# Performance work log

Hardware: AMD Instinct MI355X
Metric: run time of the kernel (lower is better)

The kernel has to match this reference:

```python
import jax, jax.numpy as jnp
import numpy as np

D_MODEL = 1024
D_STATE = 32
EXPAND = 2
D_INNER = D_MODEL * EXPAND
B_SZ = 2
SEQ = 512


def setup_inputs() -> dict:
    key = jax.random.key(0)
    ks = jax.random.split(key, 10)
    x = jax.random.normal(ks[0], (B_SZ, SEQ, D_MODEL), dtype=jnp.float32)
    W_in = jax.random.normal(ks[1], (2 * D_INNER, D_MODEL), dtype=jnp.float32) * 0.02
    A_log = jax.random.uniform(ks[2], (D_INNER, D_STATE), minval=-4.0, maxval=-1.0, dtype=jnp.float32)
    W_B = jax.random.normal(ks[3], (D_STATE, D_MODEL), dtype=jnp.float32) * 0.02
    W_C = jax.random.normal(ks[4], (D_STATE, D_MODEL), dtype=jnp.float32) * 0.02
    W_dt = jax.random.normal(ks[5], (D_INNER, D_MODEL), dtype=jnp.float32) * 0.02
    b_dt = jnp.zeros((D_INNER,), dtype=jnp.float32)
    dt_bias = jnp.zeros((D_INNER,), dtype=jnp.float32) - 4.0
    rope_freq = jax.random.normal(ks[6], (D_STATE // 2,), dtype=jnp.float32) * 0.01
    ln_w = jnp.ones((D_INNER,), dtype=jnp.float32)
    ln_b = jnp.zeros((D_INNER,), dtype=jnp.float32)
    W_out = jax.random.normal(ks[7], (D_MODEL, D_INNER), dtype=jnp.float32) * 0.02
    return {"x": x, "W_in": W_in, "A_log": A_log, "W_B": W_B, "W_C": W_C,
            "W_dt": W_dt, "b_dt": b_dt, "dt_bias": dt_bias, "rope_freq": rope_freq,
            "ln_w": ln_w, "ln_b": ln_b, "W_out": W_out}


def _forward(x, W_in, A_log, W_B, W_C, W_dt, b_dt, dt_bias, rope_freq, ln_w, ln_b, W_out):
    B, L, _ = x.shape
    half = D_STATE // 2
    offset = 0

    xz = jnp.einsum('bld,ed->ble', x, W_in)                 # [B,L,2*D_INNER]
    x_inner = xz[..., :D_INNER]                             # [B,L,DI]
    z = jax.nn.silu(xz[..., D_INNER:])                      # [B,L,DI]

    A = -jnp.exp(A_log)                                     # [DI,DS]
    Bm = jnp.einsum('bld,nd->bln', x, W_B)                  # [B,L,DS]
    Cm = jnp.einsum('bld,nd->bln', x, W_C)                  # [B,L,DS]
    dt = jax.nn.softplus(jnp.einsum('bld,ed->ble', x, W_dt) + b_dt + dt_bias)  # [B,L,DI]

    # trapezoidal discretization
    dtA = dt[..., None] * A                                 # [B,L,DI,DS]
    denom = 1.0 - dtA / 2.0
    A_bar = (1.0 + dtA / 2.0) / denom                       # [B,L,DI,DS]
    B_bar = dt[..., None] / denom                           # [B,L,DI,DS]

    # per-step rope rotation angles: angle_t = rope_freq * (t + offset)
    t_idx = jnp.arange(L, dtype=jnp.float32) + offset       # [L]
    ang = t_idx[:, None] * rope_freq                        # [L,half]
    cos_a = jnp.cos(ang)
    sin_a = jnp.sin(ang)

    def step(state, inp):
        A_t, Bb_t, B_t, x_t, C_t, c_t, s_t = inp
        # state update: [B,DI,DS]
        state = A_t * state + Bb_t * B_t[:, None, :] * x_t[:, :, None]
        real = state[..., :half]
        imag = state[..., half:]
        state = jnp.concatenate([real * c_t - imag * s_t,
                                 real * s_t + imag * c_t], axis=-1)
        y_t = jnp.einsum('bds,bs->bd', state, C_t)          # [B,DI]
        return state, y_t

    state0 = jnp.zeros((B, D_INNER, D_STATE), dtype=x.dtype)
    xs = (jnp.swapaxes(A_bar, 0, 1), jnp.swapaxes(B_bar, 0, 1),
          jnp.swapaxes(Bm, 0, 1), jnp.swapaxes(x_inner, 0, 1),
          jnp.swapaxes(Cm, 0, 1), cos_a, sin_a)
    final_state, ys = jax.lax.scan(step, state0, xs)        # ys: [L,B,DI]
    out = jnp.swapaxes(ys, 0, 1) * z                        # [B,L,DI]

    # LayerNorm over last dim (eps=1e-5, torch default)
    mu = jnp.mean(out, axis=-1, keepdims=True)
    var = jnp.mean((out - mu) ** 2, axis=-1, keepdims=True)
    out = (out - mu) * jax.lax.rsqrt(var + 1e-5) * ln_w + ln_b

    out = jnp.einsum('ble,de->bld', out, W_out)             # [B,L,D_MODEL]
    return out, final_state


def reference(x, W_in, A_log, W_B, W_C, W_dt, b_dt, dt_bias, rope_freq, ln_w, ln_b, W_out):
    return _forward(x, W_in, A_log, W_B, W_C, W_dt, b_dt, dt_bias, rope_freq, ln_w, ln_b, W_out)
```

## Files before the change

kernel.cpp:

```cpp
#include <hip/hip_runtime.h>
#include <math.h>

#define B_SZ 2
#define SEQ 512
#define DM 1024
#define DI 2048
#define DS 32
#define TOK (B_SZ*SEQ)
#define NCH 8
#define CLEN (SEQ/NCH)
#define NG (CLEN/4)
#define NPAIR (B_SZ*DI*16)

#define NFUSED 6272

__device__ __forceinline__ unsigned short f2bf(float f) {
  unsigned int u = __builtin_bit_cast(unsigned int, f);
  unsigned int r = u + 0x7fffu + ((u >> 16) & 1u);
  return (unsigned short)(r >> 16);
}

template<int CTRL>
__device__ __forceinline__ float row_ror_add(float x) {
  int s = __builtin_amdgcn_update_dpp(0, __builtin_bit_cast(int, x), CTRL, 0xf, 0xf, false);
  return x + __builtin_bit_cast(float, s);
}
__device__ __forceinline__ float row16_sum(float v) {
  v = row_ror_add<0x121>(v);
  v = row_ror_add<0x122>(v);
  v = row_ror_add<0x124>(v);
  v = row_ror_add<0x128>(v);
  return v;
}

__global__ __launch_bounds__(256) void fused_cast(const float* __restrict__ x,
                                                  const float* __restrict__ W_in,
                                                  const float* __restrict__ W_dt,
                                                  const float* __restrict__ W_B,
                                                  const float* __restrict__ W_C,
                                                  const float* __restrict__ W_out,
                                                  unsigned short* __restrict__ xb,
                                                  unsigned short* __restrict__ wcat,
                                                  unsigned short* __restrict__ wob) {
  int g = blockIdx.x * 256 + threadIdx.x;
  const float* s; unsigned short* dd; int off;
  if      (g <  131072) { s = x;     dd = xb;             off = 0; }
  else if (g <  655360) { s = W_in;  dd = wcat;           off = 131072; }
  else if (g <  917504) { s = W_dt;  dd = wcat + 4194304; off = 655360; }
  else if (g <  921600) { s = W_B;   dd = wcat + 6291456; off = 917504; }
  else if (g <  925696) { s = W_C;   dd = wcat + 6324224; off = 921600; }
  else if (g < 1187840) { s = W_out; dd = wob;            off = 925696; }
  else return;
  int i = g - off;
  float4 a = ((const float4*)s)[i * 2];
  float4 b = ((const float4*)s)[i * 2 + 1];
  union { unsigned short us[8]; uint4 v; } o;
  o.us[0] = f2bf(a.x); o.us[1] = f2bf(a.y); o.us[2] = f2bf(a.z); o.us[3] = f2bf(a.w);
  o.us[4] = f2bf(b.x); o.us[5] = f2bf(b.y); o.us[6] = f2bf(b.z); o.us[7] = f2bf(b.w);
  ((uint4*)dd)[i] = o.v;
}

typedef __attribute__((ext_vector_type(8))) short  frag8;
typedef __attribute__((ext_vector_type(4))) float  facc4;

__device__ __forceinline__ void gload_lds16(const unsigned short* g, unsigned short* l) {
  __builtin_amdgcn_global_load_lds((const __attribute__((address_space(1))) unsigned int*)g,
                                   (__attribute__((address_space(3))) unsigned int*)l, 16, 0, 0);
}

__device__ __forceinline__ float softplus_fast(float v) {
  return fmaxf(v, 0.f) + __logf(1.f + __expf(-fabsf(v)));
}

template<int BMt, int BNt, int MT, bool ROUTE>
__global__ __launch_bounds__(256) void gemm_mfma(const unsigned short* __restrict__ A,
                                                 const unsigned short* __restrict__ Bw,
                                                 int K,
                                                 float* __restrict__ o_xs,
                                                 float* __restrict__ o_zb,
                                                 float* __restrict__ o_dts,
                                                 float* __restrict__ o_bcb,
                                                 const float* __restrict__ b_dt,
                                                 const float* __restrict__ dt_bias,
                                                 float* __restrict__ o_c, int ldc) {
  constexpr int FM = BMt / 32, FN = BNt / 32;
  constexpr int IA = BMt / 64, IB = BNt / 64;
  __shared__ __align__(16) unsigned short As[BMt * 32];
  __shared__ __align__(16) unsigned short Bs[BNt * 32];
  const int tid = threadIdx.x;
  const int w = tid >> 6, lane = tid & 63;
  const int wm = w >> 1, wn = w & 1;
  const int bid = blockIdx.x;
  const int Wk = (bid & 7) * ((int)gridDim.x >> 3) + (bid >> 3);
  const int m0 = (Wk % MT) * BMt;
  const int n0 = (Wk / MT) * BNt;
  const int r = lane & 15, q = lane >> 4;
  const int grow = lane >> 2, gk = (lane & 3) * 8;
  facc4 acc[FM][FN] = {};
  const unsigned short* Ag = A + (size_t)m0 * K + gk;
  const unsigned short* Bg = Bw + (size_t)n0 * K + gk;

  for (int k0 = 0; k0 < K; k0 += 32) {
#pragma unroll
    for (int i = 0; i < IA; ++i) {
      int ch = i * 4 + w;
      gload_lds16(Ag + (size_t)(ch * 16 + grow) * K + k0, &As[ch * 512]);
    }
#pragma unroll
    for (int i = 0; i < IB; ++i) {
      int ch = i * 4 + w;
      gload_lds16(Bg + (size_t)(ch * 16 + grow) * K + k0, &Bs[ch * 512]);
    }
    __syncthreads();
    frag8 af[FM], bf[FN];
#pragma unroll
    for (int i = 0; i < FM; ++i)
      af[i] = *(const frag8*)&As[(wm * (BMt / 2) + i * 16 + r) * 32 + q * 8];
#pragma unroll
    for (int jj = 0; jj < FN; ++jj)
      bf[jj] = *(const frag8*)&Bs[(wn * (BNt / 2) + jj * 16 + r) * 32 + q * 8];
#pragma unroll
    for (int i = 0; i < FM; ++i)
#pragma unroll
      for (int jj = 0; jj < FN; ++jj)
        acc[i][jj] = __builtin_amdgcn_mfma_f32_16x16x32_bf16(af[i], bf[jj], acc[i][jj], 0, 0, 0);
    __syncthreads();
  }

#pragma unroll
  for (int i = 0; i < FM; ++i) {
#pragma unroll
    for (int jj = 0; jj < FN; ++jj) {
      int n = n0 + wn * (BNt / 2) + jj * 16 + r;
      int mb = m0 + wm * (BMt / 2) + i * 16 + q * 4;
      if (ROUTE) {
        if (n < 2048) {
#pragma unroll
          for (int rg = 0; rg < 4; ++rg)
            o_xs[(size_t)(mb + rg) * DI + n] = acc[i][jj][rg];
        } else if (n < 4096) {
#pragma unroll
          for (int rg = 0; rg < 4; ++rg)
            o_zb[(size_t)(mb + rg) * DI + (n - 2048)] = acc[i][jj][rg];
        } else if (n < 6144) {
          int d = n - 4096;
          float bias = b_dt[d] + dt_bias[d];
#pragma unroll
          for (int rg = 0; rg < 4; ++rg)
            o_dts[(size_t)(mb + rg) * DI + d] = softplus_fast(acc[i][jj][rg] + bias);
        } else if (n < 6176) {
#pragma unroll
          for (int rg = 0; rg < 4; ++rg)
            o_bcb[(size_t)(mb + rg) * DS + (n - 6144)] = acc[i][jj][rg];
        } else if (n < 6208) {
#pragma unroll
          for (int rg = 0; rg < 4; ++rg)
            o_bcb[(size_t)TOK * DS + (size_t)(mb + rg) * DS + (n - 6176)] = acc[i][jj][rg];
        }
      } else {
#pragma unroll
        for (int rg = 0; rg < 4; ++rg)
          o_c[(size_t)(mb + rg) * ldc + n] = acc[i][jj][rg];
      }
    }
  }
}


__global__ __launch_bounds__(256) void scan_p1(const float* __restrict__ xs,
                                               const float* __restrict__ dts,
                                               const float* __restrict__ bcb,
                                               const float* __restrict__ A_log,
                                               const float* __restrict__ rope,
                                               float* __restrict__ Pbuf) {
  const int blk = blockIdx.x;
  const int c = blk >> 7;
  const int sub = blk & 127;
  const int b = sub >> 6;
  const int dbase = (sub & 63) << 5;
  const int dl = threadIdx.x >> 4;
  const int j = threadIdx.x & 15;
  const int dA = dbase + dl;
  const int dB = dA + 16;
  const int l0 = c * CLEN;

  const float ArA = -0.5f * expf(A_log[dA * DS + j]);
  const float AiA = -0.5f * expf(A_log[dA * DS + j + 16]);
  const float ArB = -0.5f * expf(A_log[dB * DS + j]);
  const float AiB = -0.5f * expf(A_log[dB * DS + j + 16]);
  const float fr = rope[j];
  float sn, cs, sF, cF;
  sincosf((float)l0 * fr, &sn, &cs);
  sincosf(fr, &sF, &cF);

  const size_t base = (size_t)(b * SEQ + l0);
  const float* dtpA = dts + base * DI + dA;
  const float* xpA  = xs  + base * DI + dA;
  const float* Brp  = bcb + base * DS + j;
  const float* Bip  = Brp + 16;

  float p00A = 1.f, p01A = 0.f, p10A = 0.f, p11A = 1.f, urA = 0.f, uiA = 0.f;
  float p00B = 1.f, p01B = 0.f, p10B = 0.f, p11B = 1.f, urB = 0.f, uiB = 0.f;

  float cdtA[4], cdtB[4], cxA[4], cxB[4], cbr[4], cbi[4];
#pragma unroll
  for (int t = 0; t < 4; ++t) {
    cdtA[t] = dtpA[t * DI]; cdtB[t] = dtpA[t * DI + 16];
    cxA[t]  = xpA[t * DI];  cxB[t]  = xpA[t * DI + 16];
    cbr[t]  = Brp[t * DS];  cbi[t]  = Bip[t * DS];
  }

  for (int g = 0; g < NG; ++g) {
    const int gb = ((g + 1 < NG) ? g + 1 : g) * 4;
    float ndtA[4], ndtB[4], nxA[4], nxB[4], nbr[4], nbi[4];
#pragma unroll
    for (int t = 0; t < 4; ++t) {
      ndtA[t] = dtpA[(gb + t) * DI]; ndtB[t] = dtpA[(gb + t) * DI + 16];
      nxA[t]  = xpA[(gb + t) * DI];  nxB[t]  = xpA[(gb + t) * DI + 16];
      nbr[t]  = Brp[(gb + t) * DS];  nbi[t]  = Bip[(gb + t) * DS];
    }
#pragma unroll
    for (int t = 0; t < 4; ++t) {
      const float Br = cbr[t], Bi = cbi[t];
      {
        float dtd = cdtA[t];
        float hr = dtd * ArA, hi = dtd * AiA;
        float invr = __builtin_amdgcn_rcpf(1.f - hr);
        float invi = __builtin_amdgcn_rcpf(1.f - hi);
        float Abr = (1.f + hr) * invr;
        float Abi = (1.f + hi) * invi;
        float dx = dtd * cxA[t];
        float bxr = dx * invr * Br;
        float bxi = dx * invi * Bi;
        float tr = fmaf(Abr, urA, bxr);
        float ti = fmaf(Abi, uiA, bxi);
        urA = tr * cs - ti * sn;
        uiA = tr * sn + ti * cs;
        float q00 = Abr * p00A, q01 = Abr * p01A;
        float q10 = Abi * p10A, q11 = Abi * p11A;
        p00A = q00 * cs - q10 * sn; p10A = q00 * sn + q10 * cs;
        p01A = q01 * cs - q11 * sn; p11A = q01 * sn + q11 * cs;
      }
      {
        float dtd = cdtB[t];
        float hr = dtd * ArB, hi = dtd * AiB;
        float invr = __builtin_amdgcn_rcpf(1.f - hr);
        float invi = __builtin_amdgcn_rcpf(1.f - hi);
        float Abr = (1.f + hr) * invr;
        float Abi = (1.f + hi) * invi;
        float dx = dtd * cxB[t];
        float bxr = dx * invr * Br;
        float bxi = dx * invi * Bi;
        float tr = fmaf(Abr, urB, bxr);
        float ti = fmaf(Abi, uiB, bxi);
        urB = tr * cs - ti * sn;
        uiB = tr * sn + ti * cs;
        float q00 = Abr * p00B, q01 = Abr * p01B;
        float q10 = Abi * p10B, q11 = Abi * p11B;
        p00B = q00 * cs - q10 * sn; p10B = q00 * sn + q10 * cs;
        p01B = q01 * cs - q11 * sn; p11B = q01 * sn + q11 * cs;
      }
      float nc = fmaf(cs, cF, -sn * sF);
      float ns = fmaf(sn, cF,  cs * sF);
      cs = nc; sn = ns;
    }
#pragma unroll
    for (int t = 0; t < 4; ++t) {
      cdtA[t] = ndtA[t]; cdtB[t] = ndtB[t]; cxA[t] = nxA[t]; cxB[t] = nxB[t];
      cbr[t] = nbr[t]; cbi[t] = nbi[t];
    }
  }
  const int pairA = (b * DI + dA) * 16 + j;
  const int pairB = (b * DI + dB) * 16 + j;
  Pbuf[(c * 6 + 0) * NPAIR + pairA] = p00A;
  Pbuf[(c * 6 + 1) * NPAIR + pairA] = p01A;
  Pbuf[(c * 6 + 2) * NPAIR + pairA] = p10A;
  Pbuf[(c * 6 + 3) * NPAIR + pairA] = p11A;
  Pbuf[(c * 6 + 4) * NPAIR + pairA] = urA;
  Pbuf[(c * 6 + 5) * NPAIR + pairA] = uiA;
  Pbuf[(c * 6 + 0) * NPAIR + pairB] = p00B;
  Pbuf[(c * 6 + 1) * NPAIR + pairB] = p01B;
  Pbuf[(c * 6 + 2) * NPAIR + pairB] = p10B;
  Pbuf[(c * 6 + 3) * NPAIR + pairB] = p11B;
  Pbuf[(c * 6 + 4) * NPAIR + pairB] = urB;
  Pbuf[(c * 6 + 5) * NPAIR + pairB] = uiB;
}

__global__ __launch_bounds__(256) void scan_p3(const float* __restrict__ xs,
                                               const float* __restrict__ dts,
                                               const float* __restrict__ bcb,
                                               const float* __restrict__ A_log,
                                               const float* __restrict__ rope,
                                               const float* __restrict__ Pbuf,
                                               float* __restrict__ y,
                                               float* __restrict__ fstate) {
  const int blk = blockIdx.x;
  const int c = blk >> 7;
  const int sub = blk & 127;
  const int b = sub >> 6;
  const int dbase = (sub & 63) << 5;
  const int dl = threadIdx.x >> 4;
  const int j = threadIdx.x & 15;
  const int dA = dbase + dl;
  const int dB = dA + 16;
  const int l0 = c * CLEN;

  const float ArA = -0.5f * expf(A_log[dA * DS + j]);
  const float AiA = -0.5f * expf(A_log[dA * DS + j + 16]);
  const float ArB = -0.5f * expf(A_log[dB * DS + j]);
  const float AiB = -0.5f * expf(A_log[dB * DS + j + 16]);
  const float fr = rope[j];
  float sn, cs, sF, cF;
  sincosf((float)l0 * fr, &sn, &cs);
  sincosf(fr, &sF, &cF);

  const size_t base = (size_t)(b * SEQ + l0);
  const float* dtpA = dts + base * DI + dA;
  const float* xpA  = xs  + base * DI + dA;
  const float* Brp  = bcb + base * DS + j;
  const float* Bip  = Brp + 16;
  const float* Crp  = bcb + (size_t)TOK * DS + base * DS + j;
  const float* Cip  = Crp + 16;
  float* ypA = y + base * DI + dA;

  const int pairA = (b * DI + dA) * 16 + j;
  const int pairB = (b * DI + dB) * 16 + j;
  float srA = 0.f, siA = 0.f, srB = 0.f, siB = 0.f;
  for (int k = 0; k < c; ++k) {
    float p00 = Pbuf[(k * 6 + 0) * NPAIR + pairA];
    float p01 = Pbuf[(k * 6 + 1) * NPAIR + pairA];
    float p10 = Pbuf[(k * 6 + 2) * NPAIR + pairA];
    float p11 = Pbuf[(k * 6 + 3) * NPAIR + pairA];
    float ur  = Pbuf[(k * 6 + 4) * NPAIR + pairA];
    float ui  = Pbuf[(k * 6 + 5) * NPAIR + pairA];
    float nr = p00 * srA + p01 * siA + ur;
    float ni = p10 * srA + p11 * siA + ui;
    srA = nr; siA = ni;
    p00 = Pbuf[(k * 6 + 0) * NPAIR + pairB];
    p01 = Pbuf[(k * 6 + 1) * NPAIR + pairB];
    p10 = Pbuf[(k * 6 + 2) * NPAIR + pairB];
    p11 = Pbuf[(k * 6 + 3) * NPAIR + pairB];
    ur  = Pbuf[(k * 6 + 4) * NPAIR + pairB];
    ui  = Pbuf[(k * 6 + 5) * NPAIR + pairB];
    nr = p00 * srB + p01 * siB + ur;
    ni = p10 * srB + p11 * siB + ui;
    srB = nr; siB = ni;
  }

  float cdtA[4], cdtB[4], cxA[4], cxB[4], cbr[4], cbi[4], ccr[4], cci[4];
#pragma unroll
  for (int t = 0; t < 4; ++t) {
    cdtA[t] = dtpA[t * DI]; cdtB[t] = dtpA[t * DI + 16];
    cxA[t]  = xpA[t * DI];  cxB[t]  = xpA[t * DI + 16];
    cbr[t]  = Brp[t * DS];  cbi[t]  = Bip[t * DS];
    ccr[t]  = Crp[t * DS];  cci[t]  = Cip[t * DS];
  }

  for (int g = 0; g < NG; ++g) {
    const int gb = ((g + 1 < NG) ? g + 1 : g) * 4;
    float ndtA[4], ndtB[4], nxA[4], nxB[4], nbr[4], nbi[4], ncr[4], nci[4];
#pragma unroll
    for (int t = 0; t < 4; ++t) {
      ndtA[t] = dtpA[(gb + t) * DI]; ndtB[t] = dtpA[(gb + t) * DI + 16];
      nxA[t]  = xpA[(gb + t) * DI];  nxB[t]  = xpA[(gb + t) * DI + 16];
      nbr[t]  = Brp[(gb + t) * DS];  nbi[t]  = Bip[(gb + t) * DS];
      ncr[t]  = Crp[(gb + t) * DS];  nci[t]  = Cip[(gb + t) * DS];
    }
#pragma unroll
    for (int t = 0; t < 4; ++t) {
      const float Br = cbr[t], Bi = cbi[t], Cr = ccr[t], Ci = cci[t];
      float pA, pB;
      {
        float dtd = cdtA[t];
        float hr = dtd * ArA, hi = dtd * AiA;
        float invr = __builtin_amdgcn_rcpf(1.f - hr);
        float invi = __builtin_amdgcn_rcpf(1.f - hi);
        float Abr = (1.f + hr) * invr;
        float Abi = (1.f + hi) * invi;
        float dx = dtd * cxA[t];
        float bxr = dx * invr * Br;
        float bxi = dx * invi * Bi;
        float tr = fmaf(Abr, srA, bxr);
        float ti = fmaf(Abi, siA, bxi);
        srA = tr * cs - ti * sn;
        siA = tr * sn + ti * cs;
        pA = srA * Cr + siA * Ci;
      }
      {
        float dtd = cdtB[t];
        float hr = dtd * ArB, hi = dtd * AiB;
        float invr = __builtin_amdgcn_rcpf(1.f - hr);
        float invi = __builtin_amdgcn_rcpf(1.f - hi);
        float Abr = (1.f + hr) * invr;
        float Abi = (1.f + hi) * invi;
        float dx = dtd * cxB[t];
        float bxr = dx * invr * Br;
        float bxi = dx * invi * Bi;
        float tr = fmaf(Abr, srB, bxr);
        float ti = fmaf(Abi, siB, bxi);
        srB = tr * cs - ti * sn;
        siB = tr * sn + ti * cs;
        pB = srB * Cr + siB * Ci;
      }
      pA = row16_sum(pA);
      pB = row16_sum(pB);
      if (j == 0) {
        ypA[(g * 4 + t) * DI]      = pA;
        ypA[(g * 4 + t) * DI + 16] = pB;
      }
      float nc = fmaf(cs, cF, -sn * sF);
      float ns = fmaf(sn, cF,  cs * sF);
      cs = nc; sn = ns;
    }
#pragma unroll
    for (int t = 0; t < 4; ++t) {
      cdtA[t] = ndtA[t]; cdtB[t] = ndtB[t]; cxA[t] = nxA[t]; cxB[t] = nxB[t];
      cbr[t] = nbr[t]; cbi[t] = nbi[t]; ccr[t] = ncr[t]; cci[t] = nci[t];
    }
  }
  if (c == NCH - 1) {
    fstate[((size_t)b * DI + dA) * DS + j]      = srA;
    fstate[((size_t)b * DI + dA) * DS + j + 16] = siA;
    fstate[((size_t)b * DI + dB) * DS + j]      = srB;
    fstate[((size_t)b * DI + dB) * DS + j + 16] = siB;
  }
}

__global__ __launch_bounds__(256) void gate_ln(const float* __restrict__ y,
                                               const float* __restrict__ zb,
                                               const float* __restrict__ lw,
                                               const float* __restrict__ lb,
                                               unsigned short* __restrict__ o) {
  int tok = blockIdx.x;
  int t = threadIdx.x;
  float g[8];
  float sum = 0.f, sq = 0.f;
#pragma unroll
  for (int i = 0; i < 8; ++i) {
    int dd = t + i * 256;
    float yv = y[(size_t)tok * DI + dd];
    float zv = zb[(size_t)tok * DI + dd];
    float sg = zv / (1.f + __expf(-zv));
    float v = yv * sg;
    g[i] = v; sum += v; sq += v * v;
  }
#pragma unroll
  for (int off = 32; off; off >>= 1) { sum += __shfl_xor(sum, off); sq += __shfl_xor(sq, off); }
  __shared__ float rs[4], rq[4];
  int w = t >> 6;
  if ((t & 63) == 0) { rs[w] = sum; rq[w] = sq; }
  __syncthreads();
  sum = rs[0] + rs[1] + rs[2] + rs[3];
  sq  = rq[0] + rq[1] + rq[2] + rq[3];
  float mu = sum * (1.f / DI);
  float var = sq * (1.f / DI) - mu * mu;
  float rstd = rsqrtf(var + 1e-5f);
#pragma unroll
  for (int i = 0; i < 8; ++i) {
    int dd = t + i * 256;
    o[(size_t)tok * DI + dd] = f2bf((g[i] - mu) * rstd * lw[dd] + lb[dd]);
  }
}

extern "C" void kernel_launch(void* const* d_in, const int* in_sizes, int n_in,
                              void* d_out, int out_size, void* d_ws, size_t ws_size,
                              hipStream_t stream) {
  const float* x       = (const float*)d_in[0];
  const float* W_in    = (const float*)d_in[1];
  const float* A_log   = (const float*)d_in[2];
  const float* W_B     = (const float*)d_in[3];
  const float* W_C     = (const float*)d_in[4];
  const float* W_dt    = (const float*)d_in[5];
  const float* b_dt    = (const float*)d_in[6];
  const float* dt_bias = (const float*)d_in[7];
  const float* rope    = (const float*)d_in[8];
  const float* ln_w    = (const float*)d_in[9];
  const float* ln_b    = (const float*)d_in[10];
  const float* W_out   = (const float*)d_in[11];
  float* out = (float*)d_out;
  float* ws = (float*)d_ws;

  float* xs   = ws;
  float* zb   = ws + 2097152;
  float* dts  = ws + 4194304;
  float* bcb  = ws + 6291456;
  unsigned short* wob  = (unsigned short*)(ws + 6356992);
  unsigned short* xb   = (unsigned short*)(ws + 7405568);
  unsigned short* wcat = (unsigned short*)(ws + 7929856);
  float* Pbuf = ws + 7929856;
  float* yb   = ws + 11141120;
  unsigned short* lnb = (unsigned short*)(ws + 13238272);
  float* fstate = out + (size_t)TOK * DM;

  fused_cast<<<4640, 256, 0, stream>>>(x, W_in, W_dt, W_B, W_C, W_out, xb, wcat, wob);
  gemm_mfma<64, 64, 16, true><<<(NFUSED / 64) * (TOK / 64), 256, 0, stream>>>(
      xb, wcat, DM, xs, zb, dts, bcb, b_dt, dt_bias, nullptr, 0);
  scan_p1<<<NCH * 128, 256, 0, stream>>>(xs, dts, bcb, A_log, rope, Pbuf);
  scan_p3<<<NCH * 128, 256, 0, stream>>>(xs, dts, bcb, A_log, rope, Pbuf, yb, fstate);
  gate_ln<<<TOK, 256, 0, stream>>>(yb, zb, ln_w, ln_b, lnb);
  gemm_mfma<64, 64, 16, false><<<(DM / 64) * (TOK / 64), 256, 0, stream>>>(
      lnb, wob, DI, nullptr, nullptr, nullptr, nullptr, nullptr, nullptr, out, DM);
}
```

Baseline: 237.5 us.

## Stage scan chunk inputs into LDS via async global-to-LDS loads; skip last chunk in pass one

Both scan passes now bulk-copy their chunk's x, dt, B (and C) slices into shared memory with global_load_lds at kernel start, then iterate the recurrence from LDS instead of software-prefetching strided global loads in groups of four. The first pass also drops the final chunk's blocks, since its carry products are never consumed. This aims to replace many small strided global loads on the sequential critical path with one coalesced bulk transfer, at the cost of 24–32 KB of LDS per block, which may limit occupancy.

```diff
diff --git a/kernel.cpp b/kernel.cpp
--- a/kernel.cpp
+++ b/kernel.cpp
@@ -9,7 +9,6 @@
 #define TOK (B_SZ*SEQ)
 #define NCH 8
 #define CLEN (SEQ/NCH)
-#define NG (CLEN/4)
 #define NPAIR (B_SZ*DI*16)
 
 #define NFUSED 6272
@@ -64,6 +63,10 @@
 typedef __attribute__((ext_vector_type(4))) float  facc4;
 
 __device__ __forceinline__ void gload_lds16(const unsigned short* g, unsigned short* l) {
+  __builtin_amdgcn_global_load_lds((const __attribute__((address_space(1))) unsigned int*)g,
+                                   (__attribute__((address_space(3))) unsigned int*)l, 16, 0, 0);
+}
+__device__ __forceinline__ void gload_lds16f(const float* g, float* l) {
   __builtin_amdgcn_global_load_lds((const __attribute__((address_space(1))) unsigned int*)g,
                                    (__attribute__((address_space(3))) unsigned int*)l, 16, 0, 0);
 }
@@ -173,17 +176,36 @@
                                                const float* __restrict__ A_log,
                                                const float* __restrict__ rope,
                                                float* __restrict__ Pbuf) {
+  __shared__ __align__(16) float lds[6144];
   const int blk = blockIdx.x;
   const int c = blk >> 7;
   const int sub = blk & 127;
   const int b = sub >> 6;
   const int dbase = (sub & 63) << 5;
-  const int dl = threadIdx.x >> 4;
-  const int j = threadIdx.x & 15;
-  const int dA = dbase + dl;
+  const int tid = threadIdx.x;
+  const int wv = tid >> 6, lane = tid & 63;
+  const int dl = tid >> 4;
+  const int j = tid & 15;
+  const int l0 = c * CLEN;
+  const size_t base = (size_t)(b * SEQ + l0);
+
+  {
+    int row = wv * 16 + (lane >> 3);
+    int col = (lane & 7) << 2;
+#pragma unroll
+    for (int k = 0; k < 2; ++k) {
+      gload_lds16f(xs  + (base + row + k * 8) * DI + dbase + col, &lds[(wv * 16 + k * 8) * 32]);
+      gload_lds16f(dts + (base + row + k * 8) * DI + dbase + col, &lds[2048 + (wv * 16 + k * 8) * 32]);
+    }
+#pragma unroll
+    for (int k = 0; k < 2; ++k) {
+      int seg = wv * 2 + k;
+      gload_lds16f(bcb + base * DS + seg * 256 + lane * 4, &lds[4096 + seg * 256]);
+    }
+  }
+
+  const int dA = dbase + (dl & 15);
   const int dB = dA + 16;
-  const int l0 = c * CLEN;
-
   const float ArA = -0.5f * expf(A_log[dA * DS + j]);
   const float AiA = -0.5f * expf(A_log[dA * DS + j + 16]);
   const float ArB = -0.5f * expf(A_log[dB * DS + j]);
@@ -192,83 +214,60 @@
   float sn, cs, sF, cF;
   sincosf((float)l0 * fr, &sn, &cs);
   sincosf(fr, &sF, &cF);
-
-  const size_t base = (size_t)(b * SEQ + l0);
-  const float* dtpA = dts + base * DI + dA;
-  const float* xpA  = xs  + base * DI + dA;
-  const float* Brp  = bcb + base * DS + j;
-  const float* Bip  = Brp + 16;
+  __syncthreads();
 
   float p00A = 1.f, p01A = 0.f, p10A = 0.f, p11A = 1.f, urA = 0.f, uiA = 0.f;
   float p00B = 1.f, p01B = 0.f, p10B = 0.f, p11B = 1.f, urB = 0.f, uiB = 0.f;
-
-  float cdtA[4], cdtB[4], cxA[4], cxB[4], cbr[4], cbi[4];
-#pragma unroll
-  for (int t = 0; t < 4; ++t) {
-    cdtA[t] = dtpA[t * DI]; cdtB[t] = dtpA[t * DI + 16];
-    cxA[t]  = xpA[t * DI];  cxB[t]  = xpA[t * DI + 16];
-    cbr[t]  = Brp[t * DS];  cbi[t]  = Bip[t * DS];
-  }
-
-  for (int g = 0; g < NG; ++g) {
-    const int gb = ((g + 1 < NG) ? g + 1 : g) * 4;
-    float ndtA[4], ndtB[4], nxA[4], nxB[4], nbr[4], nbi[4];
-#pragma unroll
-    for (int t = 0; t < 4; ++t) {
-      ndtA[t] = dtpA[(gb + t) * DI]; ndtB[t] = dtpA[(gb + t) * DI + 16];
-      nxA[t]  = xpA[(gb + t) * DI];  nxB[t]  = xpA[(gb + t) * DI + 16];
-      nbr[t]  = Brp[(gb + t) * DS];  nbi[t]  = Bip[(gb + t) * DS];
-    }
-#pragma unroll
-    for (int t = 0; t < 4; ++t) {
-      const float Br = cbr[t], Bi = cbi[t];
-      {
-        float dtd = cdtA[t];
-        float hr = dtd * ArA, hi = dtd * AiA;
-        float invr = __builtin_amdgcn_rcpf(1.f - hr);
-        float invi = __builtin_amdgcn_rcpf(1.f - hi);
-        float Abr = (1.f + hr) * invr;
-        float Abi = (1.f + hi) * invi;
-        float dx = dtd * cxA[t];
-        float bxr = dx * invr * Br;
-        float bxi = dx * invi * Bi;
-        float tr = fmaf(Abr, urA, bxr);
-        float ti = fmaf(Abi, uiA, bxi);
-        urA = tr * cs - ti * sn;
-        uiA = tr * sn + ti * cs;
-        float q00 = Abr * p00A, q01 = Abr * p01A;
-        float q10 = Abi * p10A, q11 = Abi * p11A;
-        p00A = q00 * cs - q10 * sn; p10A = q00 * sn + q10 * cs;
-        p01A = q01 * cs - q11 * sn; p11A = q01 * sn + q11 * cs;
-      }
-      {
-        float dtd = cdtB[t];
-        float hr = dtd * ArB, hi = dtd * AiB;
-        float invr = __builtin_amdgcn_rcpf(1.f - hr);
-        float invi = __builtin_amdgcn_rcpf(1.f - hi);
-        float Abr = (1.f + hr) * invr;
-        float Abi = (1.f + hi) * invi;
-        float dx = dtd * cxB[t];
-        float bxr = dx * invr * Br;
-        float bxi = dx * invi * Bi;
-        float tr = fmaf(Abr, urB, bxr);
-        float ti = fmaf(Abi, uiB, bxi);
-        urB = tr * cs - ti * sn;
-        uiB = tr * sn + ti * cs;
-        float q00 = Abr * p00B, q01 = Abr * p01B;
-        float q10 = Abi * p10B, q11 = Abi * p11B;
-        p00B = q00 * cs - q10 * sn; p10B = q00 * sn + q10 * cs;
-        p01B = q01 * cs - q11 * sn; p11B = q01 * sn + q11 * cs;
-      }
-      float nc = fmaf(cs, cF, -sn * sF);
-      float ns = fmaf(sn, cF,  cs * sF);
-      cs = nc; sn = ns;
-    }
-#pragma unroll
-    for (int t = 0; t < 4; ++t) {
-      cdtA[t] = ndtA[t]; cdtB[t] = ndtB[t]; cxA[t] = nxA[t]; cxB[t] = nxB[t];
-      cbr[t] = nbr[t]; cbi[t] = nbi[t];
-    }
+  const int ca = dl & 15;
+
+#pragma unroll 4
+  for (int tt = 0; tt < CLEN; ++tt) {
+    const int ro = tt * 32;
+    float dtdA = lds[2048 + ro + ca];
+    float dtdB = lds[2048 + ro + ca + 16];
+    float xinA = lds[ro + ca];
+    float xinB = lds[ro + ca + 16];
+    float Br   = lds[4096 + ro + j];
+    float Bi   = lds[4096 + ro + j + 16];
+    {
+      float hr = dtdA * ArA, hi = dtdA * AiA;
+      float invr = __builtin_amdgcn_rcpf(1.f - hr);
+      float invi = __builtin_amdgcn_rcpf(1.f - hi);
+      float Abr = (1.f + hr) * invr;
+      float Abi = (1.f + hi) * invi;
+      float dx = dtdA * xinA;
+      float bxr = dx * invr * Br;
+      float bxi = dx * invi * Bi;
+      float tr = fmaf(Abr, urA, bxr);
+      float ti = fmaf(Abi, uiA, bxi);
+      urA = tr * cs - ti * sn;
+      uiA = tr * sn + ti * cs;
+      float q00 = Abr * p00A, q01 = Abr * p01A;
+      float q10 = Abi * p10A, q11 = Abi * p11A;
+      p00A = q00 * cs - q10 * sn; p10A = q00 * sn + q10 * cs;
+      p01A = q01 * cs - q11 * sn; p11A = q01 * sn + q11 * cs;
+    }
+    {
+      float hr = dtdB * ArB, hi = dtdB * AiB;
+      float invr = __builtin_amdgcn_rcpf(1.f - hr);
+      float invi = __builtin_amdgcn_rcpf(1.f - hi);
+      float Abr = (1.f + hr) * invr;
+      float Abi = (1.f + hi) * invi;
+      float dx = dtdB * xinB;
+      float bxr = dx * invr * Br;
+      float bxi = dx * invi * Bi;
+      float tr = fmaf(Abr, urB, bxr);
+      float ti = fmaf(Abi, uiB, bxi);
+      urB = tr * cs - ti * sn;
+      uiB = tr * sn + ti * cs;
+      float q00 = Abr * p00B, q01 = Abr * p01B;
+      float q10 = Abi * p10B, q11 = Abi * p11B;
+      p00B = q00 * cs - q10 * sn; p10B = q00 * sn + q10 * cs;
+      p01B = q01 * cs - q11 * sn; p11B = q01 * sn + q11 * cs;
+    }
+    float nc = fmaf(cs, cF, -sn * sF);
+    float ns = fmaf(sn, cF,  cs * sF);
+    cs = nc; sn = ns;
   }
   const int pairA = (b * DI + dA) * 16 + j;
   const int pairB = (b * DI + dB) * 16 + j;
@@ -294,17 +293,37 @@
                                                const float* __restrict__ Pbuf,
                                                float* __restrict__ y,
                                                float* __restrict__ fstate) {
+  __shared__ __align__(16) float lds[8192];
   const int blk = blockIdx.x;
   const int c = blk >> 7;
   const int sub = blk & 127;
   const int b = sub >> 6;
   const int dbase = (sub & 63) << 5;
-  const int dl = threadIdx.x >> 4;
-  const int j = threadIdx.x & 15;
-  const int dA = dbase + dl;
+  const int tid = threadIdx.x;
+  const int wv = tid >> 6, lane = tid & 63;
+  const int j = tid & 15;
+  const int l0 = c * CLEN;
+  const size_t base = (size_t)(b * SEQ + l0);
+
+  {
+    int row = wv * 16 + (lane >> 3);
+    int col = (lane & 7) << 2;
+#pragma unroll
+    for (int k = 0; k < 2; ++k) {
+      gload_lds16f(xs  + (base + row + k * 8) * DI + dbase + col, &lds[(wv * 16 + k * 8) * 32]);
+      gload_lds16f(dts + (base + row + k * 8) * DI + dbase + col, &lds[2048 + (wv * 16 + k * 8) * 32]);
+    }
+#pragma unroll
+    for (int k = 0; k < 2; ++k) {
+      int seg = wv * 2 + k;
+      gload_lds16f(bcb + base * DS + seg * 256 + lane * 4, &lds[4096 + seg * 256]);
+      gload_lds16f(bcb + (size_t)TOK * DS + base * DS + seg * 256 + lane * 4, &lds[6144 + seg * 256]);
+    }
+  }
+
+  const int ca = (tid >> 4) & 15;
+  const int dA = dbase + ca;
   const int dB = dA + 16;
-  const int l0 = c * CLEN;
-
   const float ArA = -0.5f * expf(A_log[dA * DS + j]);
   const float AiA = -0.5f * expf(A_log[dA * DS + j + 16]);
   const float ArB = -0.5f * expf(A_log[dB * DS + j]);
@@ -313,15 +332,6 @@
   float sn, cs, sF, cF;
   sincosf((float)l0 * fr, &sn, &cs);
   sincosf(fr, &sF, &cF);
-
-  const size_t base = (size_t)(b * SEQ + l0);
-  const float* dtpA = dts + base * DI + dA;
-  const float* xpA  = xs  + base * DI + dA;
-  const float* Brp  = bcb + base * DS + j;
-  const float* Bip  = Brp + 16;
-  const float* Crp  = bcb + (size_t)TOK * DS + base * DS + j;
-  const float* Cip  = Crp + 16;
-  float* ypA = y + base * DI + dA;
 
   const int pairA = (b * DI + dA) * 16 + j;
   const int pairB = (b * DI + dB) * 16 + j;
@@ -346,77 +356,61 @@
     ni = p10 * srB + p11 * siB + ui;
     srB = nr; siB = ni;
   }
-
-  float cdtA[4], cdtB[4], cxA[4], cxB[4], cbr[4], cbi[4], ccr[4], cci[4];
-#pragma unroll
-  for (int t = 0; t < 4; ++t) {
-    cdtA[t] = dtpA[t * DI]; cdtB[t] = dtpA[t * DI + 16];
-    cxA[t]  = xpA[t * DI];  cxB[t]  = xpA[t * DI + 16];
-    cbr[t]  = Brp[t * DS];  cbi[t]  = Bip[t * DS];
-    ccr[t]  = Crp[t * DS];  cci[t]  = Cip[t * DS];
-  }
-
-  for (int g = 0; g < NG; ++g) {
-    const int gb = ((g + 1 < NG) ? g + 1 : g) * 4;
-    float ndtA[4], ndtB[4], nxA[4], nxB[4], nbr[4], nbi[4], ncr[4], nci[4];
-#pragma unroll
-    for (int t = 0; t < 4; ++t) {
-      ndtA[t] = dtpA[(gb + t) * DI]; ndtB[t] = dtpA[(gb + t) * DI + 16];
-      nxA[t]  = xpA[(gb + t) * DI];  nxB[t]  = xpA[(gb + t) * DI + 16];
-      nbr[t]  = Brp[(gb + t) * DS];  nbi[t]  = Bip[(gb + t) * DS];
-      ncr[t]  = Crp[(gb + t) * DS];  nci[t]  = Cip[(gb + t) * DS];
-    }
-#pragma unroll
-    for (int t = 0; t < 4; ++t) {
-      const float Br = cbr[t], Bi = cbi[t], Cr = ccr[t], Ci = cci[t];
-      float pA, pB;
-      {
-        float dtd = cdtA[t];
-        float hr = dtd * ArA, hi = dtd * AiA;
-        float invr = __builtin_amdgcn_rcpf(1.f - hr);
-        float invi = __builtin_amdgcn_rcpf(1.f - hi);
-        float Abr = (1.f + hr) * invr;
-        float Abi = (1.f + hi) * invi;
-        float dx = dtd * cxA[t];
-        float bxr = dx * invr * Br;
-        float bxi = dx * invi * Bi;
-        float tr = fmaf(Abr, srA, bxr);
-        float ti = fmaf(Abi, siA, bxi);
-        srA = tr * cs - ti * sn;
-        siA = tr * sn + ti * cs;
-        pA = srA * Cr + siA * Ci;
-      }
-      {
-        float dtd = cdtB[t];
-        float hr = dtd * ArB, hi = dtd * AiB;
-        float invr = __builtin_amdgcn_rcpf(1.f - hr);
-        float invi = __builtin_amdgcn_rcpf(1.f - hi);
-        float Abr = (1.f + hr) * invr;
-        float Abi = (1.f + hi) * invi;
-        float dx = dtd * cxB[t];
-        float bxr = dx * invr * Br;
-        float bxi = dx * invi * Bi;
-        float tr = fmaf(Abr, srB, bxr);
-        float ti = fmaf(Abi, siB, bxi);
-        srB = tr * cs - ti * sn;
-        siB = tr * sn + ti * cs;
-        pB = srB * Cr + siB * Ci;
-      }
-      pA = row16_sum(pA);
-      pB = row16_sum(pB);
-      if (j == 0) {
-        ypA[(g * 4 + t) * DI]      = pA;
-        ypA[(g * 4 + t) * DI + 16] = pB;
-      }
-      float nc = fmaf(cs, cF, -sn * sF);
-      float ns = fmaf(sn, cF,  cs * sF);
-      cs = nc; sn = ns;
-    }
-#pragma unroll
-    for (int t = 0; t < 4; ++t) {
-      cdtA[t] = ndtA[t]; cdtB[t] = ndtB[t]; cxA[t] = nxA[t]; cxB[t] = nxB[t];
-      cbr[t] = nbr[t]; cbi[t] = nbi[t]; ccr[t] = ncr[t]; cci[t] = nci[t];
-    }
+  __syncthreads();
+
+  float* ypA = y + base * DI + dA;
+
+#pragma unroll 4
+  for (int tt = 0; tt < CLEN; ++tt) {
+    const int ro = tt * 32;
+    float dtdA = lds[2048 + ro + ca];
+    float dtdB = lds[2048 + ro + ca + 16];
+    float xinA = lds[ro + ca];
+    float xinB = lds[ro + ca + 16];
+    float Br   = lds[4096 + ro + j];
+    float Bi   = lds[4096 + ro + j + 16];
+    float Cr   = lds[6144 + ro + j];
+    float Ci   = lds[6144 + ro + j + 16];
+    float pA, pB;
+    {
+      float hr = dtdA * ArA, hi = dtdA * AiA;
+      float invr = __builtin_amdgcn_rcpf(1.f - hr);
+      float invi = __builtin_amdgcn_rcpf(1.f - hi);
+      float Abr = (1.f + hr) * invr;
+      float Abi = (1.f + hi) * invi;
+      float dx = dtdA * xinA;
+      float bxr = dx * invr * Br;
+      float bxi = dx * invi * Bi;
+      float tr = fmaf(Abr, srA, bxr);
+      float ti = fmaf(Abi, siA, bxi);
+      srA = tr * cs - ti * sn;
+      siA = tr * sn + ti * cs;
+      pA = srA * Cr + siA * Ci;
+    }
+    {
+      float hr = dtdB * ArB, hi = dtdB * AiB;
+      float invr = __builtin_amdgcn_rcpf(1.f - hr);
+      float invi = __builtin_amdgcn_rcpf(1.f - hi);
+      float Abr = (1.f + hr) * invr;
+      float Abi = (1.f + hi) * invi;
+      float dx = dtdB * xinB;
+      float bxr = dx * invr * Br;
+      float bxi = dx * invi * Bi;
+      float tr = fmaf(Abr, srB, bxr);
+      float ti = fmaf(Abi, siB, bxi);
+      srB = tr * cs - ti * sn;
+      siB = tr * sn + ti * cs;
+      pB = srB * Cr + siB * Ci;
+    }
+    pA = row16_sum(pA);
+    pB = row16_sum(pB);
+    if (j == 0) {
+      ypA[tt * DI]      = pA;
+      ypA[tt * DI + 16] = pB;
+    }
+    float nc = fmaf(cs, cF, -sn * sF);
+    float ns = fmaf(sn, cF,  cs * sF);
+    cs = nc; sn = ns;
   }
   if (c == NCH - 1) {
     fstate[((size_t)b * DI + dA) * DS + j]      = srA;
@@ -495,7 +489,7 @@
   fused_cast<<<4640, 256, 0, stream>>>(x, W_in, W_dt, W_B, W_C, W_out, xb, wcat, wob);
   gemm_mfma<64, 64, 16, true><<<(NFUSED / 64) * (TOK / 64), 256, 0, stream>>>(
       xb, wcat, DM, xs, zb, dts, bcb, b_dt, dt_bias, nullptr, 0);
-  scan_p1<<<NCH * 128, 256, 0, stream>>>(xs, dts, bcb, A_log, rope, Pbuf);
+  scan_p1<<<(NCH - 1) * 128, 256, 0, stream>>>(xs, dts, bcb, A_log, rope, Pbuf);
   scan_p3<<<NCH * 128, 256, 0, stream>>>(xs, dts, bcb, A_log, rope, Pbuf, yb, fstate);
   gate_ln<<<TOK, 256, 0, stream>>>(yb, zb, ln_w, ln_b, lnb);
   gemm_mfma<64, 64, 16, false><<<(DM / 64) * (TOK / 64), 256, 0, stream>>>(
```

After: 230.6 us. -2.9%, faster.
